# Kernel tuning notes

Hardware: AMD Instinct MI355X
Metric: run time of the kernel (lower is better)

## Reference

```python
import jax, jax.numpy as jnp
import numpy as np

B, NP, NC, E, C = 4, 512, 256, 128, 32
NBUCKET = 20


def soft_one_hot_linspace(x, start=0.0, end=15.0, number=NBUCKET):
    # e3nn soft_one_hot_linspace, basis='smooth_finite', cutoff=True
    values = jnp.linspace(start, end, number + 2)[1:-1]
    step = (end - start) / (number + 1)
    diff = (x[..., None] - values) / step

    def sus(y):  # exp(-1/y) for y>0 else 0 (smooth unit step)
        return jnp.where(y > 0.0, jnp.exp(-1.0 / jnp.where(y > 0.0, y, 1.0)), 0.0)

    return 1.14136 * jnp.exp(2.0) * sus(diff + 1.0) * sus(1.0 - diff)


def _init_linear(k, fan_in, fan_out):
    k1, k2 = jax.random.split(k)
    bound = 1.0 / np.sqrt(fan_in)
    W = jax.random.uniform(k1, (fan_in, fan_out), jnp.float32, -bound, bound)
    b = jax.random.uniform(k2, (fan_out,), jnp.float32, -bound, bound)
    return W, b


def setup_inputs() -> dict:
    key = jax.random.key(0)
    ks = jax.random.split(key, 12)
    inp = {}
    inp["z"] = jax.random.normal(ks[0], (B, NP, NC, E), jnp.float32)
    inp["z_mask"] = jax.random.randint(ks[1], (B, NP, NC), 0, 2) == 1
    inp["pocket_rep"] = jax.random.normal(ks[2], (B, NP, E), jnp.float32)
    inp["candidate_dis"] = jax.random.uniform(ks[3], (B, NP, NC), jnp.float32) * 16.0
    inp["W_lin"], inp["b_lin"] = _init_linear(ks[4], E, C)
    inp["W_dis"], inp["b_dis"] = _init_linear(ks[5], NBUCKET, C)
    inp["W_energy"], inp["b_energy"] = _init_linear(ks[6], C, 1)
    inp["W_gate"], inp["b_gate"] = _init_linear(ks[7], C, 1)
    inp["bias"] = jnp.ones((1,), jnp.float32)
    inp["W_energy_p"], inp["b_energy_p"] = _init_linear(ks[8], C, 1)
    inp["W_gate_p"], inp["b_gate_p"] = _init_linear(ks[9], C, 1)
    inp["bias_p"] = jnp.ones((1,), jnp.float32)
    inp["W_out"], inp["b_out"] = _init_linear(ks[10], E * C, E)
    return inp


def reference(z, z_mask, pocket_rep, candidate_dis,
              W_lin, b_lin, W_dis, b_dis,
              W_energy, b_energy, W_gate, b_gate, bias,
              W_energy_p, b_energy_p, W_gate_p, b_gate_p, bias_p,
              W_out, b_out):
    b, n_p, n_c, e = z.shape
    c = W_lin.shape[1]
    # linear + transpose(3,1): [B,Np,Nc,E] -> [B,C,Nc,Np]
    zc = jnp.transpose(z @ W_lin + b_lin, (0, 3, 2, 1))
    # softmax over last dim (Np)
    zc = jax.nn.softmax(zc, axis=-1)
    # distance-bucket bias: [B,Np,Nc,20] -> [B,Np,Nc,C] -> view [B,C,Nc,Np]
    edge_emb = soft_one_hot_linspace(candidate_dis)
    dis_bias = (edge_emb @ W_dis + b_dis).reshape(b, c, n_c, n_p)
    zc = zc + dis_bias
    # z_mask.repeat(C,1,1).view(B,C,Nc,Np) -- literal torch element order
    mask_rep = jnp.tile(z_mask, (c, 1, 1)).reshape(b, c, n_c, n_p)
    zc = jnp.where(mask_rep, jnp.asarray(1e-09, zc.dtype), zc)
    # gated energy heads on z.transpose(3,1): [B,Np,Nc,C]
    zt = jnp.transpose(zc, (0, 3, 2, 1))
    zm = z_mask.astype(zc.dtype)
    pair_energy = (jax.nn.sigmoid(zt @ W_gate + b_gate) * (zt @ W_energy + b_energy))[..., 0] * zm
    affinity_pred = jax.nn.leaky_relu(bias + pair_energy.sum(axis=(-1, -2)))
    pair_energy_p = (jax.nn.sigmoid(zt @ W_gate_p + b_gate_p) * (zt @ W_energy_p + b_energy_p))[..., 0] * zm
    prmsd_pred = jax.nn.leaky_relu(bias_p + pair_energy_p.sum(axis=(-1, -2)))
    # ligand rep: bmm([B,C*Nc,Np], [B,Np,E]) -> [B,Nc,C*E] -> Linear
    lig = jnp.einsum('bcln,bne->bcle', zc, pocket_rep)  # [B,C,Nc,E]
    lig = jnp.transpose(lig, (0, 2, 1, 3)).reshape(b, n_c, c * e)
    ligand_rep = lig @ W_out + b_out
    return (ligand_rep, affinity_pred, prmsd_pred)
```

## Files before the change

kernel.cpp:

```cpp
#include <hip/hip_runtime.h>
#include <stdint.h>


typedef float f32x4 __attribute__((ext_vector_type(4)));
typedef short s16x8 __attribute__((ext_vector_type(8)));

#define DEV static __device__ __forceinline__

DEV unsigned short f2bf(float f) {
  unsigned u = __builtin_bit_cast(unsigned, f);
  u += 0x7FFFu + ((u >> 16) & 1u);
  return (unsigned short)(u >> 16);
}
DEV float bf2f(unsigned short h) {
  unsigned u = ((unsigned)h) << 16;
  return __builtin_bit_cast(float, u);
}

__global__ void prep_k(const float* __restrict__ wlin,
                       const float* __restrict__ pocket,
                       const float* __restrict__ wout,
                       const int* __restrict__ zmask,
                       const float* __restrict__ cdis,
                       const float* __restrict__ bout,
                       unsigned short* __restrict__ wtlin,
                       unsigned short* __restrict__ pt,
                       unsigned short* __restrict__ wto,
                       unsigned long long* __restrict__ zmb,
                       float* __restrict__ cdisT,
                       float* __restrict__ outp,
                       float* __restrict__ accg) {
  for (int i = blockIdx.x * 256 + threadIdx.x; i < 1970184; i += gridDim.x * 256) {
    if (i < 524288) {
      int np = i & 511, nc = (i >> 9) & 255, b = i >> 17;
      unsigned long long bal = __ballot(zmask[b * 131072 + np * 256 + nc] != 0);
      if ((i & 63) == 0) zmb[i >> 6] = bal;
    } else if (i < 1048576) {
      int o = i - 524288;
      int e = o >> 12, k = o & 4095;
      wto[o] = f2bf(wout[k * 128 + e]);
    } else if (i < 1310720) {
      int o = i - 1048576;
      int np = o & 511, r = o >> 9;
      int e = r & 127, b = r >> 7;
      pt[o] = f2bf(pocket[(b * 512 + np) * 128 + e]);
    } else if (i < 1314816) {
      int o = i - 1310720;
      int k = o & 127, c = o >> 7;
      wtlin[o] = f2bf(wlin[k * 32 + c]);
    } else if (i < 1314824) {
      accg[i - 1314816] = 0.0f;
    } else if (i < 1839112) {
      int o = i - 1314824;
      int c = o & 31, np5 = (o >> 5) & 15, nc = (o >> 9) & 255, b = o >> 17;
      cdisT[o] = cdis[(b * 512 + 16 * c + (nc >> 4)) * 256 + 16 * (nc & 15) + np5];
    } else {
      int o = i - 1839112;
      outp[o] = bout[o & 127];
    }
  }
}

extern __shared__ char smem[];

__global__ __launch_bounds__(256, 4) void mega_k(
    const float* __restrict__ z, const int* __restrict__ zmask,
    const float* __restrict__ cdisT,
    const float* __restrict__ wdis, const float* __restrict__ bdis_g,
    const float* __restrict__ wE, const float* __restrict__ bE,
    const float* __restrict__ wG, const float* __restrict__ bG,
    const float* __restrict__ wEp, const float* __restrict__ bEp,
    const float* __restrict__ wGp, const float* __restrict__ bGp,
    const unsigned short* __restrict__ wtlin,
    const unsigned short* __restrict__ pt,
    const unsigned long long* __restrict__ zmb,
    unsigned short* __restrict__ lig, float* __restrict__ accg) {
  const int nc = blockIdx.x, b = blockIdx.y;
  const int t = threadIdx.x;
  const int w = t >> 6, ln = t & 63;
  const int m16 = ln & 15, q = ln >> 4;

  unsigned short* T = (unsigned short*)smem;

  __shared__ float s_wd[640];
  __shared__ float s_bd[32];
  __shared__ float s_we[32], s_wg[32], s_wep[32], s_wgp[32];
  __shared__ float s_red[160];
  __shared__ float s_gmax[32], s_gsum[32];
  __shared__ unsigned long long s_mb[4][8];
  __shared__ float s_r8[8];

  if (t < 32) {
    s_bd[t] = bdis_g[t];
    s_we[t] = wE[t]; s_wg[t] = wG[t];
    s_wep[t] = wEp[t]; s_wgp[t] = wGp[t];
  }
  for (int i = t; i < 640; i += 256) s_wd[i] = wdis[i];
  for (int i = t; i < 2048; i += 256) {
    int cm = i >> 9, nn = i & 511;
    unsigned long long bal = __ballot(zmask[cm * 131072 + nc * 512 + nn] != 0);
    if ((i & 63) == 0) s_mb[cm][nn >> 6] = bal;
  }

  f32x4 acc1[8][2];
#pragma unroll
  for (int i = 0; i < 8; ++i) {
    acc1[i][0] = f32x4{0.f, 0.f, 0.f, 0.f};
    acc1[i][1] = f32x4{0.f, 0.f, 0.f, 0.f};
  }
  const float* zb = z + (size_t)b * 16777216 + (size_t)nc * 128;
  for (int k0 = 0; k0 < 128; k0 += 32) {
    s16x8 bf0 = *(const s16x8*)(wtlin + m16 * 128 + k0 + q * 8);
    s16x8 bf1 = *(const s16x8*)(wtlin + (16 + m16) * 128 + k0 + q * 8);
#pragma unroll
    for (int bt = 0; bt < 4; ++bt) {
      f32x4 z0[2], z1[2];
#pragma unroll
      for (int i = 0; i < 2; ++i) {
        int np = (w * 8 + bt * 2 + i) * 16 + m16;
        const float* p = zb + (size_t)np * 32768 + k0 + q * 8;
        z0[i] = *(const f32x4*)p;
        z1[i] = *(const f32x4*)(p + 4);
      }
#pragma unroll
      for (int i = 0; i < 2; ++i) {
        s16x8 af;
        af[0] = (short)f2bf(z0[i][0]); af[1] = (short)f2bf(z0[i][1]);
        af[2] = (short)f2bf(z0[i][2]); af[3] = (short)f2bf(z0[i][3]);
        af[4] = (short)f2bf(z1[i][0]); af[5] = (short)f2bf(z1[i][1]);
        af[6] = (short)f2bf(z1[i][2]); af[7] = (short)f2bf(z1[i][3]);
        int ai = bt * 2 + i;
        acc1[ai][0] = __builtin_amdgcn_mfma_f32_16x16x32_bf16(af, bf0, acc1[ai][0], 0, 0, 0);
        acc1[ai][1] = __builtin_amdgcn_mfma_f32_16x16x32_bf16(af, bf1, acc1[ai][1], 0, 0, 0);
      }
    }
  }

  float mx[2] = {-3.0e38f, -3.0e38f};
#pragma unroll
  for (int ai = 0; ai < 8; ++ai)
#pragma unroll
    for (int ct = 0; ct < 2; ++ct)
#pragma unroll
      for (int r = 0; r < 4; ++r) mx[ct] = fmaxf(mx[ct], acc1[ai][ct][r]);
#pragma unroll
  for (int ct = 0; ct < 2; ++ct) {
    float v = mx[ct];
    v = fmaxf(v, __shfl_xor(v, 16));
    v = fmaxf(v, __shfl_xor(v, 32));
    mx[ct] = v;
  }
  if (ln < 16) { s_red[ln * 5 + w] = mx[0]; s_red[(16 + ln) * 5 + w] = mx[1]; }
  __syncthreads();
  if (t < 32)
    s_gmax[t] = fmaxf(fmaxf(s_red[t * 5], s_red[t * 5 + 1]),
                      fmaxf(s_red[t * 5 + 2], s_red[t * 5 + 3]));
  __syncthreads();
  float sm[2] = {0.f, 0.f};
#pragma unroll
  for (int ct = 0; ct < 2; ++ct) {
    float g = s_gmax[ct * 16 + m16];
#pragma unroll
    for (int ai = 0; ai < 8; ++ai)
#pragma unroll
      for (int r = 0; r < 4; ++r) {
        float e = __expf(acc1[ai][ct][r] - g);
        acc1[ai][ct][r] = e;
        sm[ct] += e;
      }
  }
#pragma unroll
  for (int ct = 0; ct < 2; ++ct) {
    float v = sm[ct];
    v += __shfl_xor(v, 16);
    v += __shfl_xor(v, 32);
    sm[ct] = v;
  }
  if (ln < 16) { s_red[ln * 5 + w] = sm[0]; s_red[(16 + ln) * 5 + w] = sm[1]; }
  __syncthreads();
  if (t < 32)
    s_gsum[t] = 1.0f / (s_red[t * 5] + s_red[t * 5 + 1] + s_red[t * 5 + 2] + s_red[t * 5 + 3]);
  __syncthreads();

#pragma unroll
  for (int ct = 0; ct < 2; ++ct) {
    int c = ct * 16 + m16;
    float s = s_gsum[c];
#pragma unroll
    for (int ai = 0; ai < 8; ++ai) {
      int npb = (w * 8 + ai) * 16 + q * 4;
      unsigned lo = (unsigned)f2bf(acc1[ai][ct][0] * s) |
                    ((unsigned)f2bf(acc1[ai][ct][1] * s) << 16);
      unsigned hi = (unsigned)f2bf(acc1[ai][ct][2] * s) |
                    ((unsigned)f2bf(acc1[ai][ct][3] * s) << 16);
      *(uint2*)(T + c * 520 + npb) = make_uint2(lo, hi);
    }
  }
  __syncthreads();

  {
    const float SUSK = 8.4335794f;
    const float* cdb = cdisT + (size_t)(b * 256 + nc) * 512;
#pragma unroll
    for (int tt = 0; tt < 2; ++tt) {
      int task = t + tt * 256;
      int c = task & 31, np5 = task >> 5;
      float d = cdb[task];
      float val[32];
#pragma unroll
      for (int kk = 0; kk < 32; ++kk) val[kk] = s_bd[kk];
      for (int j = 0; j < 20; ++j) {
        float diff = d * (21.0f / 15.0f) - (float)(j + 1);
        float y1 = diff + 1.f, y2 = 1.f - diff;
        float u = 0.f;
        if (y1 > 0.f && y2 > 0.f) u = SUSK * __expf(-1.f / y1 - 1.f / y2);
#pragma unroll
        for (int kk = 0; kk < 32; ++kk) val[kk] += u * s_wd[j * 32 + kk];
      }
      int npb = np5 * 32;
      unsigned long long mw = s_mb[c & 3][npb >> 6];
#pragma unroll
      for (int kb2 = 0; kb2 < 4; ++kb2) {
        unsigned short* tp = T + c * 520 + npb + kb2 * 8;
        s16x8 tv = *(s16x8*)tp;
        s16x8 ov;
#pragma unroll
        for (int kk = 0; kk < 8; ++kk) {
          float x = bf2f((unsigned short)tv[kk]) + val[kb2 * 8 + kk];
          int mk = (int)((mw >> ((npb + kb2 * 8 + kk) & 63)) & 1ull);
          ov[kk] = (short)f2bf(mk ? 1e-9f : x);
        }
        *(s16x8*)tp = ov;
      }
    }
  }
  __syncthreads();

  {
    float aff = 0.f, prm = 0.f;
    const float bg0 = bG[0], be0 = bE[0], bgp0 = bGp[0], bep0 = bEp[0];
    const unsigned long long* zw = zmb + (size_t)(b * 256 + nc) * 8;
#pragma unroll
    for (int s = 0; s < 2; ++s) {
      int np = s * 256 + t;
      float g = bg0, e = be0, gp = bgp0, ep = bep0;
      for (int c = 0; c < 32; ++c) {
        float tv = bf2f(T[c * 520 + np]);
        g += tv * s_wg[c]; e += tv * s_we[c];
        gp += tv * s_wgp[c]; ep += tv * s_wep[c];
      }
      if ((zw[np >> 6] >> (np & 63)) & 1ull) {
        aff += e / (1.f + __expf(-g));
        prm += ep / (1.f + __expf(-gp));
      }
    }
#pragma unroll
    for (int d = 32; d >= 1; d >>= 1) {
      aff += __shfl_xor(aff, d);
      prm += __shfl_xor(prm, d);
    }
    if (ln == 0) { s_r8[w] = aff; s_r8[4 + w] = prm; }
    __syncthreads();
    if (t == 0) {
      atomicAdd(accg + b, s_r8[0] + s_r8[1] + s_r8[2] + s_r8[3]);
      atomicAdd(accg + 4 + b, s_r8[4] + s_r8[5] + s_r8[6] + s_r8[7]);
    }
  }

  {
    f32x4 a5[2][2];
    a5[0][0] = f32x4{0.f, 0.f, 0.f, 0.f}; a5[0][1] = a5[0][0];
    a5[1][0] = a5[0][0]; a5[1][1] = a5[0][0];
    const unsigned short* ptb = pt + b * 65536;
    for (int k0 = 0; k0 < 512; k0 += 32) {
      s16x8 aT0 = *(const s16x8*)(T + m16 * 520 + k0 + q * 8);
      s16x8 aT1 = *(const s16x8*)(T + (16 + m16) * 520 + k0 + q * 8);
      s16x8 bP0 = *(const s16x8*)(ptb + (w * 32 + m16) * 512 + k0 + q * 8);
      s16x8 bP1 = *(const s16x8*)(ptb + (w * 32 + 16 + m16) * 512 + k0 + q * 8);
      a5[0][0] = __builtin_amdgcn_mfma_f32_16x16x32_bf16(aT0, bP0, a5[0][0], 0, 0, 0);
      a5[0][1] = __builtin_amdgcn_mfma_f32_16x16x32_bf16(aT0, bP1, a5[0][1], 0, 0, 0);
      a5[1][0] = __builtin_amdgcn_mfma_f32_16x16x32_bf16(aT1, bP0, a5[1][0], 0, 0, 0);
      a5[1][1] = __builtin_amdgcn_mfma_f32_16x16x32_bf16(aT1, bP1, a5[1][1], 0, 0, 0);
    }
    unsigned short* lg = lig + (size_t)(b * 256 + nc) * 4096;
#pragma unroll
    for (int mt = 0; mt < 2; ++mt)
#pragma unroll
      for (int u = 0; u < 2; ++u)
#pragma unroll
        for (int r = 0; r < 4; ++r) {
          int c = mt * 16 + q * 4 + r;
          int e = w * 32 + u * 16 + m16;
          lg[c * 128 + e] = f2bf(a5[mt][u][r]);
        }
  }
}

__global__ __launch_bounds__(256, 2) void proj_k(
    const unsigned short* __restrict__ lig, const unsigned short* __restrict__ wto,
    const float* __restrict__ accg, const float* __restrict__ bias,
    const float* __restrict__ biasp, float* __restrict__ outp) {
  const int mb = blockIdx.x, ks = blockIdx.y;
  const int t = threadIdx.x, w = t >> 6, ln = t & 63;
  const int m16 = ln & 15, q = ln >> 4;
  f32x4 acc[2][8];
#pragma unroll
  for (int mt = 0; mt < 2; ++mt)
#pragma unroll
    for (int nt = 0; nt < 8; ++nt) acc[mt][nt] = f32x4{0.f, 0.f, 0.f, 0.f};
  const int kb = ks * 256;
  for (int k0 = 0; k0 < 256; k0 += 32) {
    s16x8 af[2], bf[8];
#pragma unroll
    for (int mt = 0; mt < 2; ++mt)
      af[mt] = *(const s16x8*)(lig + (size_t)(mb * 128 + (w * 2 + mt) * 16 + m16) * 4096 + kb + k0 + q * 8);
#pragma unroll
    for (int nt = 0; nt < 8; ++nt)
      bf[nt] = *(const s16x8*)(wto + (size_t)(nt * 16 + m16) * 4096 + kb + k0 + q * 8);
#pragma unroll
    for (int mt = 0; mt < 2; ++mt)
#pragma unroll
      for (int nt = 0; nt < 8; ++nt)
        acc[mt][nt] = __builtin_amdgcn_mfma_f32_16x16x32_bf16(af[mt], bf[nt], acc[mt][nt], 0, 0, 0);
  }
#pragma unroll
  for (int mt = 0; mt < 2; ++mt)
#pragma unroll
    for (int nt = 0; nt < 8; ++nt)
#pragma unroll
      for (int r = 0; r < 4; ++r)
        atomicAdd(outp + (size_t)(mb * 128 + (w * 2 + mt) * 16 + q * 4 + r) * 128 + nt * 16 + m16,
                  acc[mt][nt][r]);
  if (mb == 0 && ks == 0 && t < 8) {
    float base = (t < 4) ? bias[0] : biasp[0];
    float x = base + accg[t];
    outp[131072 + t] = (x >= 0.f) ? x : 0.01f * x;
  }
}

extern "C" void kernel_launch(void* const* d_in, const int* in_sizes, int n_in,
                              void* d_out, int out_size, void* d_ws, size_t ws_size,
                              hipStream_t stream) {
  const float* z      = (const float*)d_in[0];
  const int*   zmask  = (const int*)d_in[1];
  const float* pocket = (const float*)d_in[2];
  const float* cdis   = (const float*)d_in[3];
  const float* wlin   = (const float*)d_in[4];
  const float* wdis   = (const float*)d_in[6];
  const float* bdis   = (const float*)d_in[7];
  const float* wE     = (const float*)d_in[8];
  const float* bE     = (const float*)d_in[9];
  const float* wG     = (const float*)d_in[10];
  const float* bG     = (const float*)d_in[11];
  const float* bias   = (const float*)d_in[12];
  const float* wEp    = (const float*)d_in[13];
  const float* bEp    = (const float*)d_in[14];
  const float* wGp    = (const float*)d_in[15];
  const float* bGp    = (const float*)d_in[16];
  const float* biasp  = (const float*)d_in[17];
  const float* wout   = (const float*)d_in[18];
  const float* bout   = (const float*)d_in[19];

  char* ws = (char*)d_ws;
  float* accg                  = (float*)(ws + 0);
  unsigned short* wtlin        = (unsigned short*)(ws + 1024);
  unsigned long long* zmb      = (unsigned long long*)(ws + 16384);
  unsigned short* pt           = (unsigned short*)(ws + 131072);
  float* cdisT                 = (float*)(ws + 655360);
  unsigned short* wto          = (unsigned short*)(ws + 2752512);
  unsigned short* lig          = (unsigned short*)(ws + 4194304);
  float* outp = (float*)d_out;

  prep_k<<<1024, 256, 0, stream>>>(wlin, pocket, wout, zmask, cdis, bout,
                                   wtlin, pt, wto, zmb, cdisT, outp, accg);
  mega_k<<<dim3(256, 4), 256, 33280, stream>>>(z, zmask, cdisT, wdis, bdis,
      wE, bE, wG, bG, wEp, bEp, wGp, bGp, wtlin, pt, zmb, lig, accg);
  proj_k<<<dim3(8, 16), 256, 0, stream>>>(lig, wto, accg, bias, biasp, outp);
}
```

Before: 471.0 us.

## Precompute mask bits in prep, tile-transpose W_out, split-K projection with reduce kernel

The W_out transpose moves out of the strided prep loop into a tiled shared-memory transpose kernel, so its reads are coalesced. The per-block zmask ballot in the main kernel is replaced by a mask bitmap that prep builds once; the main kernel loads it, plus its own row of zmb, into shared memory. The projection now writes split-K partials to a workspace instead of issuing fp32 atomics, and a new reduce kernel sums them and adds the bias. This adds two kernel launches and extra workspace traffic, and the main kernel's launch bound drops from 4 to 3 blocks per SM.

Result: slower. 486.2 us (+3.2%).

```diff
diff --git a/kernel.cpp b/kernel.cpp
--- a/kernel.cpp
+++ b/kernel.cpp
@@ -19,30 +19,27 @@
 
 __global__ void prep_k(const float* __restrict__ wlin,
                        const float* __restrict__ pocket,
-                       const float* __restrict__ wout,
                        const int* __restrict__ zmask,
                        const float* __restrict__ cdis,
-                       const float* __restrict__ bout,
                        unsigned short* __restrict__ wtlin,
                        unsigned short* __restrict__ pt,
-                       unsigned short* __restrict__ wto,
                        unsigned long long* __restrict__ zmb,
+                       unsigned long long* __restrict__ smb,
                        float* __restrict__ cdisT,
-                       float* __restrict__ outp,
                        float* __restrict__ accg) {
-  for (int i = blockIdx.x * 256 + threadIdx.x; i < 1970184; i += gridDim.x * 256) {
+  for (int i = blockIdx.x * 256 + threadIdx.x; i < 1839112; i += gridDim.x * 256) {
     if (i < 524288) {
       int np = i & 511, nc = (i >> 9) & 255, b = i >> 17;
       unsigned long long bal = __ballot(zmask[b * 131072 + np * 256 + nc] != 0);
       if ((i & 63) == 0) zmb[i >> 6] = bal;
     } else if (i < 1048576) {
       int o = i - 524288;
-      int e = o >> 12, k = o & 4095;
-      wto[o] = f2bf(wout[k * 128 + e]);
+      int nn = o & 511, cm = (o >> 9) & 3, nc = o >> 11;
+      unsigned long long bal = __ballot(zmask[cm * 131072 + nc * 512 + nn] != 0);
+      if ((o & 63) == 0) smb[o >> 6] = bal;
     } else if (i < 1310720) {
       int o = i - 1048576;
-      int np = o & 511, r = o >> 9;
-      int e = r & 127, b = r >> 7;
+      int np = o & 511, e = (o >> 9) & 127, b = o >> 16;
       pt[o] = f2bf(pocket[(b * 512 + np) * 128 + e]);
     } else if (i < 1314816) {
       int o = i - 1310720;
@@ -50,21 +47,37 @@
       wtlin[o] = f2bf(wlin[k * 32 + c]);
     } else if (i < 1314824) {
       accg[i - 1314816] = 0.0f;
-    } else if (i < 1839112) {
+    } else {
       int o = i - 1314824;
       int c = o & 31, np5 = (o >> 5) & 15, nc = (o >> 9) & 255, b = o >> 17;
       cdisT[o] = cdis[(b * 512 + 16 * c + (nc >> 4)) * 256 + 16 * (nc & 15) + np5];
-    } else {
-      int o = i - 1839112;
-      outp[o] = bout[o & 127];
-    }
+    }
+  }
+}
+
+__global__ void tr_k(const float* __restrict__ wout,
+                     unsigned short* __restrict__ wto) {
+  __shared__ float tile[64][65];
+  const int kt = blockIdx.x, et = blockIdx.y;
+  const int t = threadIdx.x;
+  const int col = t & 63, r0 = t >> 6;
+#pragma unroll
+  for (int rr = 0; rr < 16; ++rr) {
+    int row = rr * 4 + r0;
+    tile[row][col] = wout[(kt * 64 + row) * 128 + et * 64 + col];
+  }
+  __syncthreads();
+#pragma unroll
+  for (int rr = 0; rr < 16; ++rr) {
+    int erow = rr * 4 + r0;
+    wto[(et * 64 + erow) * 4096 + kt * 64 + col] = f2bf(tile[col][erow]);
   }
 }
 
 extern __shared__ char smem[];
 
-__global__ __launch_bounds__(256, 4) void mega_k(
-    const float* __restrict__ z, const int* __restrict__ zmask,
+__global__ __launch_bounds__(256, 3) void mega_k(
+    const float* __restrict__ z,
     const float* __restrict__ cdisT,
     const float* __restrict__ wdis, const float* __restrict__ bdis_g,
     const float* __restrict__ wE, const float* __restrict__ bE,
@@ -74,6 +87,7 @@
     const unsigned short* __restrict__ wtlin,
     const unsigned short* __restrict__ pt,
     const unsigned long long* __restrict__ zmb,
+    const unsigned long long* __restrict__ smb,
     unsigned short* __restrict__ lig, float* __restrict__ accg) {
   const int nc = blockIdx.x, b = blockIdx.y;
   const int t = threadIdx.x;
@@ -88,19 +102,17 @@
   __shared__ float s_red[160];
   __shared__ float s_gmax[32], s_gsum[32];
   __shared__ unsigned long long s_mb[4][8];
+  __shared__ unsigned long long s_zw[8];
   __shared__ float s_r8[8];
 
   if (t < 32) {
     s_bd[t] = bdis_g[t];
     s_we[t] = wE[t]; s_wg[t] = wG[t];
     s_wep[t] = wEp[t]; s_wgp[t] = wGp[t];
-  }
+    s_mb[t >> 3][t & 7] = smb[nc * 32 + t];
+  }
+  if (t >= 32 && t < 40) s_zw[t - 32] = zmb[(b * 256 + nc) * 8 + (t - 32)];
   for (int i = t; i < 640; i += 256) s_wd[i] = wdis[i];
-  for (int i = t; i < 2048; i += 256) {
-    int cm = i >> 9, nn = i & 511;
-    unsigned long long bal = __ballot(zmask[cm * 131072 + nc * 512 + nn] != 0);
-    if ((i & 63) == 0) s_mb[cm][nn >> 6] = bal;
-  }
 
   f32x4 acc1[8][2];
 #pragma unroll
@@ -239,7 +251,6 @@
   {
     float aff = 0.f, prm = 0.f;
     const float bg0 = bG[0], be0 = bE[0], bgp0 = bGp[0], bep0 = bEp[0];
-    const unsigned long long* zw = zmb + (size_t)(b * 256 + nc) * 8;
 #pragma unroll
     for (int s = 0; s < 2; ++s) {
       int np = s * 256 + t;
@@ -249,7 +260,7 @@
         g += tv * s_wg[c]; e += tv * s_we[c];
         gp += tv * s_wgp[c]; ep += tv * s_wep[c];
       }
-      if ((zw[np >> 6] >> (np & 63)) & 1ull) {
+      if ((s_zw[np >> 6] >> (np & 63)) & 1ull) {
         aff += e / (1.f + __expf(-g));
         prm += ep / (1.f + __expf(-gp));
       }
@@ -298,43 +309,46 @@
 
 __global__ __launch_bounds__(256, 2) void proj_k(
     const unsigned short* __restrict__ lig, const unsigned short* __restrict__ wto,
-    const float* __restrict__ accg, const float* __restrict__ bias,
-    const float* __restrict__ biasp, float* __restrict__ outp) {
+    float* __restrict__ part) {
   const int mb = blockIdx.x, ks = blockIdx.y;
   const int t = threadIdx.x, w = t >> 6, ln = t & 63;
   const int m16 = ln & 15, q = ln >> 4;
-  f32x4 acc[2][8];
-#pragma unroll
-  for (int mt = 0; mt < 2; ++mt)
-#pragma unroll
-    for (int nt = 0; nt < 8; ++nt) acc[mt][nt] = f32x4{0.f, 0.f, 0.f, 0.f};
-  const int kb = ks * 256;
-  for (int k0 = 0; k0 < 256; k0 += 32) {
-    s16x8 af[2], bf[8];
-#pragma unroll
-    for (int mt = 0; mt < 2; ++mt)
-      af[mt] = *(const s16x8*)(lig + (size_t)(mb * 128 + (w * 2 + mt) * 16 + m16) * 4096 + kb + k0 + q * 8);
+  f32x4 acc[8];
+#pragma unroll
+  for (int nt = 0; nt < 8; ++nt) acc[nt] = f32x4{0.f, 0.f, 0.f, 0.f};
+  const int kb = ks * 512;
+  const int row = mb * 64 + w * 16 + m16;
+  for (int k0 = 0; k0 < 512; k0 += 32) {
+    s16x8 af = *(const s16x8*)(lig + (size_t)row * 4096 + kb + k0 + q * 8);
+    s16x8 bf[8];
 #pragma unroll
     for (int nt = 0; nt < 8; ++nt)
       bf[nt] = *(const s16x8*)(wto + (size_t)(nt * 16 + m16) * 4096 + kb + k0 + q * 8);
 #pragma unroll
-    for (int mt = 0; mt < 2; ++mt)
-#pragma unroll
-      for (int nt = 0; nt < 8; ++nt)
-        acc[mt][nt] = __builtin_amdgcn_mfma_f32_16x16x32_bf16(af[mt], bf[nt], acc[mt][nt], 0, 0, 0);
-  }
-#pragma unroll
-  for (int mt = 0; mt < 2; ++mt)
-#pragma unroll
     for (int nt = 0; nt < 8; ++nt)
-#pragma unroll
-      for (int r = 0; r < 4; ++r)
-        atomicAdd(outp + (size_t)(mb * 128 + (w * 2 + mt) * 16 + q * 4 + r) * 128 + nt * 16 + m16,
-                  acc[mt][nt][r]);
-  if (mb == 0 && ks == 0 && t < 8) {
-    float base = (t < 4) ? bias[0] : biasp[0];
-    float x = base + accg[t];
-    outp[131072 + t] = (x >= 0.f) ? x : 0.01f * x;
+      acc[nt] = __builtin_amdgcn_mfma_f32_16x16x32_bf16(af, bf[nt], acc[nt], 0, 0, 0);
+  }
+  float* pp = part + (size_t)ks * 131072 + (size_t)(mb * 64 + w * 16) * 128;
+#pragma unroll
+  for (int nt = 0; nt < 8; ++nt)
+#pragma unroll
+    for (int r = 0; r < 4; ++r)
+      pp[(q * 4 + r) * 128 + nt * 16 + m16] = acc[nt][r];
+}
+
+__global__ void reduce_k(const float* __restrict__ part, const float* __restrict__ bout,
+                         const float* __restrict__ accg, const float* __restrict__ bias,
+                         const float* __restrict__ biasp, float* __restrict__ outp) {
+  int i = blockIdx.x * 256 + threadIdx.x;
+  float s = bout[i & 127];
+#pragma unroll
+  for (int ks = 0; ks < 8; ++ks) s += part[(size_t)ks * 131072 + i];
+  outp[i] = s;
+  if (blockIdx.x == 0 && threadIdx.x < 8) {
+    int tt = threadIdx.x;
+    float base = (tt < 4) ? bias[0] : biasp[0];
+    float x = base + accg[tt];
+    outp[131072 + tt] = (x >= 0.f) ? x : 0.01f * x;
   }
 }
 
@@ -365,15 +379,19 @@
   float* accg                  = (float*)(ws + 0);
   unsigned short* wtlin        = (unsigned short*)(ws + 1024);
   unsigned long long* zmb      = (unsigned long long*)(ws + 16384);
-  unsigned short* pt           = (unsigned short*)(ws + 131072);
-  float* cdisT                 = (float*)(ws + 655360);
-  unsigned short* wto          = (unsigned short*)(ws + 2752512);
+  unsigned long long* smb      = (unsigned long long*)(ws + 81920);
+  unsigned short* pt           = (unsigned short*)(ws + 393216);
+  float* cdisT                 = (float*)(ws + 1048576);
+  unsigned short* wto          = (unsigned short*)(ws + 3145728);
   unsigned short* lig          = (unsigned short*)(ws + 4194304);
+  float* part                  = (float*)(ws + 12582912);
   float* outp = (float*)d_out;
 
-  prep_k<<<1024, 256, 0, stream>>>(wlin, pocket, wout, zmask, cdis, bout,
-                                   wtlin, pt, wto, zmb, cdisT, outp, accg);
-  mega_k<<<dim3(256, 4), 256, 33280, stream>>>(z, zmask, cdisT, wdis, bdis,
-      wE, bE, wG, bG, wEp, bEp, wGp, bGp, wtlin, pt, zmb, lig, accg);
-  proj_k<<<dim3(8, 16), 256, 0, stream>>>(lig, wto, accg, bias, biasp, outp);
-}
+  prep_k<<<1024, 256, 0, stream>>>(wlin, pocket, zmask, cdis,
+                                   wtlin, pt, zmb, smb, cdisT, accg);
+  tr_k<<<dim3(64, 2), 256, 0, stream>>>(wout, wto);
+  mega_k<<<dim3(256, 4), 256, 33280, stream>>>(z, cdisT, wdis, bdis,
+      wE, bE, wG, bG, wEp, bEp, wGp, bGp, wtlin, pt, zmb, smb, lig, accg);
+  proj_k<<<dim3(16, 8), 256, 0, stream>>>(lig, wto, part);
+  reduce_k<<<512, 256, 0, stream>>>(part, bout, accg, bias, biasp, outp);
+}
```
